# Performance work log

Hardware: AMD Instinct MI355X
Metric: run time of the kernel (lower is better)

The kernel has to match this reference:

```python
import jax, jax.numpy as jnp
import numpy as np

N, B, T, D = 4, 4, 512, 512
H, DK, DV = 8, 64, 64
LN_EPS = 1e-5


def setup_inputs() -> dict:
    key = jax.random.key(0)
    ks = jax.random.split(key, 5)
    s = 1.0 / np.sqrt(D)
    return {
        "x": jax.random.normal(ks[0], (N, B, T, D), jnp.float32),
        "Wq": jax.random.normal(ks[1], (D, H * DK), jnp.float32) * s,
        "bq": jnp.zeros((H * DK,), jnp.float32),
        "Wk": jax.random.normal(ks[2], (D, H * DK), jnp.float32) * s,
        "bk": jnp.zeros((H * DK,), jnp.float32),
        "Wv": jax.random.normal(ks[3], (D, H * DV), jnp.float32) * s,
        "bv": jnp.zeros((H * DV,), jnp.float32),
        "Wo": jax.random.normal(ks[4], (H * DV, D), jnp.float32) * (1.0 / np.sqrt(H * DV)),
        "bo": jnp.zeros((D,), jnp.float32),
        "gamma": jnp.ones((D,), jnp.float32),
        "beta": jnp.zeros((D,), jnp.float32),
    }


def reference(x, Wq, bq, Wk, bk, Wv, bv, Wo, bo, gamma, beta):
    # x: [N, B, T, D] -- N variables, each [B, T, D]
    n = x.shape[0]
    # Project once per variable (the torch code redundantly recomputes K/V per query var).
    q = (x @ Wq + bq).reshape(n, B, T, H, DK).transpose(0, 1, 3, 2, 4)  # [N,B,H,T,DK]
    k = (x @ Wk + bk).reshape(n, B, T, H, DK).transpose(0, 1, 3, 2, 4)  # [N,B,H,T,DK]
    v = (x @ Wv + bv).reshape(n, B, T, H, DV).transpose(0, 1, 3, 2, 4)  # [N,B,H,T,DV]
    # All-pairs attention: softmax over keys of EACH key-variable separately.
    scores = jnp.einsum('qbhtk,cbhsk->qcbhts', q, k) / np.sqrt(DK)  # [Nq,Nc,B,H,T,T]
    attn = jax.nn.softmax(scores, axis=-1)
    ctx = jnp.einsum('qcbhts,cbhsv->qcbhtv', attn, v)  # [Nq,Nc,B,H,T,DV]
    ctx = ctx.transpose(0, 1, 2, 4, 3, 5).reshape(n, n, B, T, H * DV)
    out = ctx @ Wo + bo                     # per-pair output projection
    out = out.sum(axis=1) / n               # average over key variables -> [N,B,T,D]
    res = x + out
    mu = res.mean(axis=-1, keepdims=True)
    var = res.var(axis=-1, keepdims=True)
    y = (res - mu) / jnp.sqrt(var + LN_EPS) * gamma + beta
    return y
```

## Files before the change

### kernel.cpp

```cpp
#include <hip/hip_runtime.h>


typedef __bf16 bf16x8 __attribute__((ext_vector_type(8)));
typedef __bf16 bf16x4 __attribute__((ext_vector_type(4)));
typedef short shortx4 __attribute__((ext_vector_type(4)));
typedef float floatx2 __attribute__((ext_vector_type(2)));
typedef float floatx4 __attribute__((ext_vector_type(4)));
typedef float floatx16 __attribute__((ext_vector_type(16)));
typedef unsigned short ushortx8 __attribute__((ext_vector_type(8)));
typedef unsigned int uintx4 __attribute__((ext_vector_type(4)));

static __device__ __forceinline__ unsigned short f2bf(float f) {
  union { __bf16 h; unsigned short u; } c; c.h = (__bf16)f; return c.u;
}
static __device__ __forceinline__ float bf2f(unsigned short u) {
  union { unsigned u32; float f; } c; c.u32 = ((unsigned)u) << 16; return c.f;
}
static __device__ __forceinline__ unsigned cvtpk(float a, float b) {
  unsigned r;
  asm("v_cvt_pk_bf16_f32 %0, %1, %2" : "=v"(r) : "v"(a), "v"(b));
  return r;
}

#define QSCALE 0.18033688011112042f
#define SHIFT2 (-17.312340489609306f)

__global__ __launch_bounds__(256) void prep(
    const float* __restrict__ Wq, const float* __restrict__ Wk,
    const float* __restrict__ Wv, const float* __restrict__ Wo,
    const float* __restrict__ x,
    unsigned short* __restrict__ wqkvT, unsigned short* __restrict__ woT,
    unsigned short* __restrict__ x_bf)
{
  const int bid = blockIdx.x;
  const int tid = threadIdx.x;
  if (bid < 256) {
    __shared__ unsigned short lds[64][65];
    const int z = bid >> 6, rest = bid & 63;
    const int k0 = (rest >> 3) * 64, n0 = (rest & 7) * 64;
    const float* W; unsigned short* T;
    if (z == 0)      { W = Wq; T = wqkvT; }
    else if (z == 1) { W = Wk; T = wqkvT + 262144; }
    else if (z == 2) { W = Wv; T = wqkvT + 524288; }
    else             { W = Wo; T = woT; }
    const int xx = tid & 63, yy = tid >> 6;
#pragma unroll
    for (int i = 0; i < 16; ++i) {
      const int row = yy * 16 + i;
      lds[row][xx] = f2bf(W[(size_t)(k0 + row) * 512 + n0 + xx]);
    }
    __syncthreads();
#pragma unroll
    for (int i = 0; i < 16; ++i) {
      const int nr = yy * 16 + i;
      T[(size_t)(n0 + nr) * 512 + k0 + xx] = lds[xx][nr];
    }
  } else {
    const int i = (bid - 256) * 256 + tid;
    const float4 a = ((const float4*)x)[i * 2];
    const float4 b = ((const float4*)x)[i * 2 + 1];
    ushortx8 o;
    o[0] = f2bf(a.x); o[1] = f2bf(a.y); o[2] = f2bf(a.z); o[3] = f2bf(a.w);
    o[4] = f2bf(b.x); o[5] = f2bf(b.y); o[6] = f2bf(b.z); o[7] = f2bf(b.w);
    *(ushortx8*)(x_bf + (size_t)i * 8) = o;
  }
}

__global__ __launch_bounds__(256) void gemm_qkv(
    const unsigned short* __restrict__ Xb,
    const unsigned short* __restrict__ BT,
    const float* __restrict__ bq, const float* __restrict__ bk,
    const float* __restrict__ bv,
    unsigned short* __restrict__ Qo, unsigned short* __restrict__ Ko,
    unsigned short* __restrict__ Vo)
{
  __shared__ __align__(16) unsigned short sbuf[18432];
  auto lA = (unsigned short (*)[72])sbuf;
  auto lB = (unsigned short (*)[72])(sbuf + 9216);
  const int tid  = threadIdx.x;
  const int wv   = tid >> 6, lane = tid & 63;
  const int quad = lane >> 4, l16 = lane & 15;
  const int wm = wv >> 1, wn = wv & 1;
  const int m0  = blockIdx.x * 128;
  const int n0g = blockIdx.y * 128;
  const int sel = n0g >> 9;
  const float* bias = (sel == 0) ? bq : (sel == 1) ? bk : bv;
  const float scale = (sel == 0) ? QSCALE : 1.0f;
  unsigned short* outp = (sel == 0) ? Qo : (sel == 1) ? Ko : Vo;

  floatx4 acc[4][4] = {};
  const int srow = tid >> 1, sc0 = (tid & 1) * 32;

  for (int kc = 0; kc < 512; kc += 64) {
    __syncthreads();
    const unsigned short* as = Xb + (size_t)(m0 + srow) * 512 + kc + sc0;
    const unsigned short* bs = BT + (size_t)(n0g + srow) * 512 + kc + sc0;
#pragma unroll
    for (int j = 0; j < 4; ++j) {
      *(bf16x8*)&lA[srow][sc0 + j * 8] = *(const bf16x8*)(as + j * 8);
      *(bf16x8*)&lB[srow][sc0 + j * 8] = *(const bf16x8*)(bs + j * 8);
    }
    __syncthreads();
    bf16x8 af[4][2];
#pragma unroll
    for (int ti = 0; ti < 4; ++ti) {
      af[ti][0] = *(const bf16x8*)&lA[wm * 64 + ti * 16 + l16][quad * 8];
      af[ti][1] = *(const bf16x8*)&lA[wm * 64 + ti * 16 + l16][32 + quad * 8];
    }
#pragma unroll
    for (int ni = 0; ni < 4; ++ni) {
      bf16x8 b0 = *(const bf16x8*)&lB[wn * 64 + ni * 16 + l16][quad * 8];
      bf16x8 b1 = *(const bf16x8*)&lB[wn * 64 + ni * 16 + l16][32 + quad * 8];
#pragma unroll
      for (int ti = 0; ti < 4; ++ti) {
        acc[ti][ni] = __builtin_amdgcn_mfma_f32_16x16x32_bf16(af[ti][0], b0, acc[ti][ni], 0, 0, 0);
        acc[ti][ni] = __builtin_amdgcn_mfma_f32_16x16x32_bf16(af[ti][1], b1, acc[ti][ni], 0, 0, 0);
      }
    }
  }

  __syncthreads();
  if (sel != 2) {
    auto tb = (unsigned short (*)[136])sbuf;
#pragma unroll
    for (int ni = 0; ni < 4; ++ni) {
      const int ncol = wn * 64 + ni * 16 + l16;
      const float bvv = bias[(n0g & 511) + ncol];
#pragma unroll
      for (int ti = 0; ti < 4; ++ti) {
        const int mrow = wm * 64 + ti * 16 + quad * 4;
#pragma unroll
        for (int r = 0; r < 4; ++r)
          tb[mrow + r][ncol] = f2bf((acc[ti][ni][r] + bvv) * scale);
      }
    }
    __syncthreads();
    const int mrow = tid >> 1, th = tid & 1;
    const int m = m0 + mrow;
    const int nb2 = m >> 9, t = m & 511;
    const int hh = ((n0g & 511) >> 6) + th;
    unsigned short* gdst = outp + ((size_t)(nb2 * 8 + hh) * 512 + t) * 64;
#pragma unroll
    for (int j = 0; j < 8; ++j)
      *(ushortx8*)(gdst + j * 8) = *(const ushortx8*)&tb[mrow][th * 64 + j * 8];
  } else {
    auto tb = (unsigned short (*)[136])sbuf;
#pragma unroll
    for (int ni = 0; ni < 4; ++ni) {
      const int n = (n0g & 511) + wn * 64 + ni * 16 + l16;
      const float bvv = bias[n];
      const int drow = wn * 64 + ni * 16 + l16;
#pragma unroll
      for (int ti = 0; ti < 4; ++ti) {
        const int tcol = wm * 64 + ti * 16 + quad * 4;
        shortx4 pk;
        pk[0] = (short)f2bf(acc[ti][ni][0] + bvv);
        pk[1] = (short)f2bf(acc[ti][ni][1] + bvv);
        pk[2] = (short)f2bf(acc[ti][ni][2] + bvv);
        pk[3] = (short)f2bf(acc[ti][ni][3] + bvv);
        *(shortx4*)&tb[drow][tcol] = pk;
      }
    }
    __syncthreads();
    const int drow = tid >> 1, th = tid & 1;
    const int n = (n0g & 511) + drow;
    const int hh = n >> 6, dk = n & 63;
    const int nb = m0 >> 9, tbase = (m0 & 511) + th * 64;
    unsigned short* gdst = outp + ((size_t)(nb * 8 + hh) * 64 + dk) * 512 + tbase;
#pragma unroll
    for (int j = 0; j < 8; ++j)
      *(ushortx8*)(gdst + j * 8) = *(const ushortx8*)&tb[drow][th * 64 + j * 8];
  }
}

__global__ __launch_bounds__(256) void gemm_out(
    const unsigned short* __restrict__ C0, const unsigned short* __restrict__ C1,
    const unsigned short* __restrict__ BT, unsigned short* __restrict__ Cout)
{
  __shared__ __align__(16) unsigned short sbuf[18432];
  auto lA = (unsigned short (*)[72])sbuf;
  auto lB = (unsigned short (*)[72])(sbuf + 9216);
  const int tid  = threadIdx.x;
  const int wv   = tid >> 6, lane = tid & 63;
  const int quad = lane >> 4, l16 = lane & 15;
  const int wm = wv >> 1, wn = wv & 1;
  const int m0 = blockIdx.x * 128, n0 = blockIdx.y * 128;

  floatx4 acc[4][4] = {};
  const int srow = tid >> 1, sc0 = (tid & 1) * 32;

  for (int kc = 0; kc < 512; kc += 64) {
    __syncthreads();
    const size_t aoff = (size_t)(m0 + srow) * 512 + kc + sc0;
    const unsigned short* bs = BT + (size_t)(n0 + srow) * 512 + kc + sc0;
#pragma unroll
    for (int j = 0; j < 4; ++j) {
      ushortx8 a0 = *(const ushortx8*)(C0 + aoff + j * 8);
      ushortx8 a1 = *(const ushortx8*)(C1 + aoff + j * 8);
      ushortx8 o;
#pragma unroll
      for (int e = 0; e < 8; ++e) o[e] = f2bf(bf2f(a0[e]) + bf2f(a1[e]));
      *(ushortx8*)&lA[srow][sc0 + j * 8] = o;
      *(bf16x8*)&lB[srow][sc0 + j * 8] = *(const bf16x8*)(bs + j * 8);
    }
    __syncthreads();
    bf16x8 af[4][2];
#pragma unroll
    for (int ti = 0; ti < 4; ++ti) {
      af[ti][0] = *(const bf16x8*)&lA[wm * 64 + ti * 16 + l16][quad * 8];
      af[ti][1] = *(const bf16x8*)&lA[wm * 64 + ti * 16 + l16][32 + quad * 8];
    }
#pragma unroll
    for (int ni = 0; ni < 4; ++ni) {
      bf16x8 b0 = *(const bf16x8*)&lB[wn * 64 + ni * 16 + l16][quad * 8];
      bf16x8 b1 = *(const bf16x8*)&lB[wn * 64 + ni * 16 + l16][32 + quad * 8];
#pragma unroll
      for (int ti = 0; ti < 4; ++ti) {
        acc[ti][ni] = __builtin_amdgcn_mfma_f32_16x16x32_bf16(af[ti][0], b0, acc[ti][ni], 0, 0, 0);
        acc[ti][ni] = __builtin_amdgcn_mfma_f32_16x16x32_bf16(af[ti][1], b1, acc[ti][ni], 0, 0, 0);
      }
    }
  }

  __syncthreads();
  auto tb = (unsigned short (*)[136])sbuf;
#pragma unroll
  for (int ni = 0; ni < 4; ++ni) {
    const int ncol = wn * 64 + ni * 16 + l16;
#pragma unroll
    for (int ti = 0; ti < 4; ++ti) {
      const int mrow = wm * 64 + ti * 16 + quad * 4;
#pragma unroll
      for (int r = 0; r < 4; ++r)
        tb[mrow + r][ncol] = f2bf(acc[ti][ni][r]);
    }
  }
  __syncthreads();
  const int mrow = tid >> 1, th = tid & 1;
  unsigned short* gdst = Cout + (size_t)(m0 + mrow) * 512 + n0 + th * 64;
#pragma unroll
  for (int j = 0; j < 8; ++j)
    *(ushortx8*)(gdst + j * 8) = *(const ushortx8*)&tb[mrow][th * 64 + j * 8];
}

__global__ __launch_bounds__(256) void flash_kernel(
    const unsigned short* __restrict__ Q,
    const unsigned short* __restrict__ K,
    const unsigned short* __restrict__ VT,
    unsigned short* __restrict__ CTX2)
{
  __shared__ __align__(16) unsigned short lK[2][64][72];
  __shared__ __align__(16) unsigned short lV[2][64][68];
  const int tid  = threadIdx.x;
  const int wv   = tid >> 6, lane = tid & 63;
  const int l32  = lane & 31, u = lane >> 5;

  const int lin  = blockIdx.x;
  const int xcd  = lin & 7, slot = lin >> 3;
  const int tile = slot & 3;
  const int nbh  = xcd * 16 + ((slot >> 2) & 15);
  const int cg   = slot >> 6;
  const int t0   = tile * 128;
  const int h = nbh & 7, nb = nbh >> 3, b = nb & 3;

  const unsigned short* qbase = Q + ((size_t)nbh * 512 + (t0 + wv * 32 + l32)) * 64;
  bf16x8 qf[4];
#pragma unroll
  for (int c16 = 0; c16 < 4; ++c16)
    qf[c16] = *(const bf16x8*)(qbase + c16 * 16 + u * 8);

  const int srow = tid >> 2, sc0 = (tid & 3) * 16;
  const unsigned short *kptr, *vptr;
  auto setptr = [&](int it) {
    const int c = cg * 2 + (it >> 3), s0 = (it & 7) * 64;
    const size_t kvbh = (size_t)((c * 4 + b) * 8 + h);
    kptr = K  + kvbh * (512 * 64) + (size_t)(s0 + srow) * 64 + sc0;
    vptr = VT + kvbh * (64 * 512) + (size_t)srow * 512 + s0 + sc0;
  };
  bf16x8 rk0, rk1, rv0, rv1;
  auto loadregs = [&]() {
    rk0 = *(const bf16x8*)kptr; rk1 = *(const bf16x8*)(kptr + 8);
    rv0 = *(const bf16x8*)vptr; rv1 = *(const bf16x8*)(vptr + 8);
  };
  auto writebuf = [&](int p) {
    *(bf16x8*)&lK[p][srow][sc0]     = rk0;
    *(bf16x8*)&lK[p][srow][sc0 + 8] = rk1;
    union { bf16x8 v8; bf16x4 v4[2]; } c0, c1;
    c0.v8 = rv0; c1.v8 = rv1;
    *(bf16x4*)&lV[p][srow][sc0]      = c0.v4[0];
    *(bf16x4*)&lV[p][srow][sc0 + 4]  = c0.v4[1];
    *(bf16x4*)&lV[p][srow][sc0 + 8]  = c1.v4[0];
    *(bf16x4*)&lV[p][srow][sc0 + 12] = c1.v4[1];
  };

  setptr(0); loadregs();
  writebuf(0);
  setptr(1); loadregs();
  __syncthreads();

  floatx16 ofin0 = {}, ofin1 = {};
  floatx16 oc0, oc1;
  floatx2 lac2;

  for (int it = 0; it < 16; ++it) {
    const int cur = it & 1;
    const int st = it & 7;
    if (st == 0) { oc0 = floatx16{}; oc1 = floatx16{}; lac2 = floatx2{}; }

    if (it < 15) writebuf(cur ^ 1);
    if (it < 14) { setptr(it + 2); loadregs(); }

    __builtin_amdgcn_s_setprio(1);
    floatx16 sacc0, sacc1;
#pragma unroll
    for (int r = 0; r < 16; ++r) { sacc0[r] = SHIFT2; sacc1[r] = SHIFT2; }
#pragma unroll
    for (int c16 = 0; c16 < 4; ++c16) {
      bf16x8 ak0 = *(const bf16x8*)&lK[cur][l32][c16 * 16 + u * 8];
      bf16x8 ak1 = *(const bf16x8*)&lK[cur][32 + l32][c16 * 16 + u * 8];
      sacc0 = __builtin_amdgcn_mfma_f32_32x32x16_bf16(ak0, qf[c16], sacc0, 0, 0, 0);
      sacc1 = __builtin_amdgcn_mfma_f32_32x32x16_bf16(ak1, qf[c16], sacc1, 0, 0, 0);
    }

#pragma unroll
    for (int sb = 0; sb < 2; ++sb) {
      const floatx16& sa = sb ? sacc1 : sacc0;
#pragma unroll
      for (int g = 0; g < 2; ++g) {
        float e[8];
#pragma unroll
        for (int j = 0; j < 8; ++j) e[j] = __builtin_amdgcn_exp2f(sa[8 * g + j]);
        floatx2 s01 = floatx2{e[0], e[1]} + floatx2{e[2], e[3]};
        floatx2 s23 = floatx2{e[4], e[5]} + floatx2{e[6], e[7]};
        lac2 += s01 + s23;
        union { unsigned u32[4]; bf16x8 b8; } pf;
        pf.u32[0] = cvtpk(e[0], e[1]);
        pf.u32[1] = cvtpk(e[2], e[3]);
        pf.u32[2] = cvtpk(e[4], e[5]);
        pf.u32[3] = cvtpk(e[6], e[7]);
        const int slA = sb * 32 + g * 16 + u * 4;
        union { shortx4 s4[2]; bf16x8 b8; } va, vb;
        va.s4[0] = *(const shortx4*)&lV[cur][l32][slA];
        va.s4[1] = *(const shortx4*)&lV[cur][l32][slA + 8];
        vb.s4[0] = *(const shortx4*)&lV[cur][32 + l32][slA];
        vb.s4[1] = *(const shortx4*)&lV[cur][32 + l32][slA + 8];
        oc0 = __builtin_amdgcn_mfma_f32_32x32x16_bf16(pf.b8, va.b8, oc0, 0, 0, 0);
        oc1 = __builtin_amdgcn_mfma_f32_32x32x16_bf16(pf.b8, vb.b8, oc1, 0, 0, 0);
      }
    }
    __builtin_amdgcn_s_setprio(0);

    if (st == 7) {
      float s = lac2[0] + lac2[1];
      s += __shfl_xor(s, 32);
      const float inv = 1.0f / s;
#pragma unroll
      for (int r = 0; r < 16; ++r) {
        const int trow = (r & 3) + 8 * (r >> 2) + 4 * u;
        const float invr = __shfl(inv, trow);
        ofin0[r] += oc0[r] * invr;
        ofin1[r] += oc1[r] * invr;
      }
    }
    __syncthreads();
  }

  unsigned short* outp = CTX2 + (size_t)cg * (8192 * 512);
  const int mbase = nb * 512 + t0 + wv * 32;
#pragma unroll
  for (int r = 0; r < 16; ++r) {
    const int trow = (r & 3) + 8 * (r >> 2) + 4 * u;
    const size_t rowoff = (size_t)(mbase + trow) * 512 + h * 64;
    outp[rowoff + l32]      = f2bf(ofin0[r]);
    outp[rowoff + 32 + l32] = f2bf(ofin1[r]);
  }
}

__global__ __launch_bounds__(256) void ln_kernel(
    const float* __restrict__ x, const unsigned short* __restrict__ tmpb,
    const float* __restrict__ bo, const float* __restrict__ gamma,
    const float* __restrict__ beta, float* __restrict__ out)
{
  const int wv   = threadIdx.x >> 6, lane = threadIdx.x & 63;
  const int row  = blockIdx.x * 4 + wv;
  const int col  = lane * 8;
  const size_t base = (size_t)row * 512 + col;
  const float4 x0 = *(const float4*)(x + base);
  const float4 x1 = *(const float4*)(x + base + 4);
  const ushortx8 t8 = *(const ushortx8*)(tmpb + base);
  const float4 b0 = *(const float4*)(bo + col);
  const float4 b1 = *(const float4*)(bo + col + 4);
  float r[8];
  r[0] = x0.x + 0.25f * bf2f(t8[0]) + b0.x;  r[1] = x0.y + 0.25f * bf2f(t8[1]) + b0.y;
  r[2] = x0.z + 0.25f * bf2f(t8[2]) + b0.z;  r[3] = x0.w + 0.25f * bf2f(t8[3]) + b0.w;
  r[4] = x1.x + 0.25f * bf2f(t8[4]) + b1.x;  r[5] = x1.y + 0.25f * bf2f(t8[5]) + b1.y;
  r[6] = x1.z + 0.25f * bf2f(t8[6]) + b1.z;  r[7] = x1.w + 0.25f * bf2f(t8[7]) + b1.w;
  float s = 0.f, sq = 0.f;
#pragma unroll
  for (int j = 0; j < 8; ++j) { s += r[j]; sq += r[j] * r[j]; }
#pragma unroll
  for (int off = 1; off < 64; off <<= 1) {
    s  += __shfl_xor(s, off);
    sq += __shfl_xor(sq, off);
  }
  const float mu  = s * (1.0f / 512.0f);
  const float var = sq * (1.0f / 512.0f) - mu * mu;
  const float inv = rsqrtf(var + 1e-5f);
  const float4 g0 = *(const float4*)(gamma + col);
  const float4 g1 = *(const float4*)(gamma + col + 4);
  const float4 be0 = *(const float4*)(beta + col);
  const float4 be1 = *(const float4*)(beta + col + 4);
  float4 o0, o1;
  o0.x = (r[0] - mu) * inv * g0.x + be0.x;  o0.y = (r[1] - mu) * inv * g0.y + be0.y;
  o0.z = (r[2] - mu) * inv * g0.z + be0.z;  o0.w = (r[3] - mu) * inv * g0.w + be0.w;
  o1.x = (r[4] - mu) * inv * g1.x + be1.x;  o1.y = (r[5] - mu) * inv * g1.y + be1.y;
  o1.z = (r[6] - mu) * inv * g1.z + be1.z;  o1.w = (r[7] - mu) * inv * g1.w + be1.w;
  *(float4*)(out + base)     = o0;
  *(float4*)(out + base + 4) = o1;
}

extern "C" void kernel_launch(void* const* d_in, const int* in_sizes, int n_in,
                              void* d_out, int out_size, void* d_ws, size_t ws_size,
                              hipStream_t stream) {
  const float* x     = (const float*)d_in[0];
  const float* Wq    = (const float*)d_in[1];
  const float* bq    = (const float*)d_in[2];
  const float* Wk    = (const float*)d_in[3];
  const float* bk    = (const float*)d_in[4];
  const float* Wv    = (const float*)d_in[5];
  const float* bv    = (const float*)d_in[6];
  const float* Wo    = (const float*)d_in[7];
  const float* bo    = (const float*)d_in[8];
  const float* gamma = (const float*)d_in[9];
  const float* beta  = (const float*)d_in[10];
  float* out = (float*)d_out;

  char* w = (char*)d_ws;
  unsigned short* q_bf  = (unsigned short*)(w);
  unsigned short* k_bf  = (unsigned short*)(w + (size_t)8  * 1024 * 1024);
  unsigned short* vt_bf = (unsigned short*)(w + (size_t)16 * 1024 * 1024);
  unsigned short* x_bf  = (unsigned short*)(w + (size_t)24 * 1024 * 1024);
  unsigned short* ctx2  = (unsigned short*)(w + (size_t)24 * 1024 * 1024);
  unsigned short* wqkvT = (unsigned short*)(w + (size_t)40 * 1024 * 1024);
  unsigned short* woT   = wqkvT + 786432;
  unsigned short* tmpb  = (unsigned short*)(w);

  prep<<<2304, 256, 0, stream>>>(Wq, Wk, Wv, Wo, x, wqkvT, woT, x_bf);
  gemm_qkv<<<dim3(64, 12), 256, 0, stream>>>(x_bf, wqkvT, bq, bk, bv,
                                             q_bf, k_bf, vt_bf);
  flash_kernel<<<1024, 256, 0, stream>>>(q_bf, k_bf, vt_bf, ctx2);
  gemm_out<<<dim3(64, 4), 256, 0, stream>>>(ctx2, ctx2 + (size_t)8192 * 512,
                                            woT, tmpb);
  ln_kernel<<<2048, 256, 0, stream>>>(x, tmpb, bo, gamma, beta, out);
}
```

Measured before the change: 185.5 us.

## Fuse output projection GEMM with residual add and LayerNorm

Replaces the separate output-projection GEMM and LayerNorm kernels with one kernel. Each 512-thread block computes a full 64-row by 512-column output tile into shared memory, then applies the residual, bias and LayerNorm directly. This removes the bf16 intermediate write and read and one kernel launch. In exchange the grid shrinks to 128 blocks, which leaves many CUs idle. The A-operand sum is also recomputed for each of the four column chunks.

```diff
diff --git a/kernel.cpp b/kernel.cpp
--- a/kernel.cpp
+++ b/kernel.cpp
@@ -171,76 +171,6 @@
     for (int j = 0; j < 8; ++j)
       *(ushortx8*)(gdst + j * 8) = *(const ushortx8*)&tb[drow][th * 64 + j * 8];
   }
-}
-
-__global__ __launch_bounds__(256) void gemm_out(
-    const unsigned short* __restrict__ C0, const unsigned short* __restrict__ C1,
-    const unsigned short* __restrict__ BT, unsigned short* __restrict__ Cout)
-{
-  __shared__ __align__(16) unsigned short sbuf[18432];
-  auto lA = (unsigned short (*)[72])sbuf;
-  auto lB = (unsigned short (*)[72])(sbuf + 9216);
-  const int tid  = threadIdx.x;
-  const int wv   = tid >> 6, lane = tid & 63;
-  const int quad = lane >> 4, l16 = lane & 15;
-  const int wm = wv >> 1, wn = wv & 1;
-  const int m0 = blockIdx.x * 128, n0 = blockIdx.y * 128;
-
-  floatx4 acc[4][4] = {};
-  const int srow = tid >> 1, sc0 = (tid & 1) * 32;
-
-  for (int kc = 0; kc < 512; kc += 64) {
-    __syncthreads();
-    const size_t aoff = (size_t)(m0 + srow) * 512 + kc + sc0;
-    const unsigned short* bs = BT + (size_t)(n0 + srow) * 512 + kc + sc0;
-#pragma unroll
-    for (int j = 0; j < 4; ++j) {
-      ushortx8 a0 = *(const ushortx8*)(C0 + aoff + j * 8);
-      ushortx8 a1 = *(const ushortx8*)(C1 + aoff + j * 8);
-      ushortx8 o;
-#pragma unroll
-      for (int e = 0; e < 8; ++e) o[e] = f2bf(bf2f(a0[e]) + bf2f(a1[e]));
-      *(ushortx8*)&lA[srow][sc0 + j * 8] = o;
-      *(bf16x8*)&lB[srow][sc0 + j * 8] = *(const bf16x8*)(bs + j * 8);
-    }
-    __syncthreads();
-    bf16x8 af[4][2];
-#pragma unroll
-    for (int ti = 0; ti < 4; ++ti) {
-      af[ti][0] = *(const bf16x8*)&lA[wm * 64 + ti * 16 + l16][quad * 8];
-      af[ti][1] = *(const bf16x8*)&lA[wm * 64 + ti * 16 + l16][32 + quad * 8];
-    }
-#pragma unroll
-    for (int ni = 0; ni < 4; ++ni) {
-      bf16x8 b0 = *(const bf16x8*)&lB[wn * 64 + ni * 16 + l16][quad * 8];
-      bf16x8 b1 = *(const bf16x8*)&lB[wn * 64 + ni * 16 + l16][32 + quad * 8];
-#pragma unroll
-      for (int ti = 0; ti < 4; ++ti) {
-        acc[ti][ni] = __builtin_amdgcn_mfma_f32_16x16x32_bf16(af[ti][0], b0, acc[ti][ni], 0, 0, 0);
-        acc[ti][ni] = __builtin_amdgcn_mfma_f32_16x16x32_bf16(af[ti][1], b1, acc[ti][ni], 0, 0, 0);
-      }
-    }
-  }
-
-  __syncthreads();
-  auto tb = (unsigned short (*)[136])sbuf;
-#pragma unroll
-  for (int ni = 0; ni < 4; ++ni) {
-    const int ncol = wn * 64 + ni * 16 + l16;
-#pragma unroll
-    for (int ti = 0; ti < 4; ++ti) {
-      const int mrow = wm * 64 + ti * 16 + quad * 4;
-#pragma unroll
-      for (int r = 0; r < 4; ++r)
-        tb[mrow + r][ncol] = f2bf(acc[ti][ni][r]);
-    }
-  }
-  __syncthreads();
-  const int mrow = tid >> 1, th = tid & 1;
-  unsigned short* gdst = Cout + (size_t)(m0 + mrow) * 512 + n0 + th * 64;
-#pragma unroll
-  for (int j = 0; j < 8; ++j)
-    *(ushortx8*)(gdst + j * 8) = *(const ushortx8*)&tb[mrow][th * 64 + j * 8];
 }
 
 __global__ __launch_bounds__(256) void flash_kernel(
@@ -376,47 +306,111 @@
   }
 }
 
-__global__ __launch_bounds__(256) void ln_kernel(
-    const float* __restrict__ x, const unsigned short* __restrict__ tmpb,
-    const float* __restrict__ bo, const float* __restrict__ gamma,
-    const float* __restrict__ beta, float* __restrict__ out)
+__global__ __launch_bounds__(512) void gemm_out_ln(
+    const unsigned short* __restrict__ C0, const unsigned short* __restrict__ C1,
+    const unsigned short* __restrict__ BT,
+    const float* __restrict__ x, const float* __restrict__ bo,
+    const float* __restrict__ gamma, const float* __restrict__ beta,
+    float* __restrict__ out)
 {
-  const int wv   = threadIdx.x >> 6, lane = threadIdx.x & 63;
-  const int row  = blockIdx.x * 4 + wv;
-  const int col  = lane * 8;
-  const size_t base = (size_t)row * 512 + col;
-  const float4 x0 = *(const float4*)(x + base);
-  const float4 x1 = *(const float4*)(x + base + 4);
-  const ushortx8 t8 = *(const ushortx8*)(tmpb + base);
+  __shared__ __align__(16) unsigned short outbuf[64][520];
+  __shared__ __align__(16) unsigned short lA[64][72];
+  __shared__ __align__(16) unsigned short lB[128][72];
+  const int tid  = threadIdx.x;
+  const int wv   = tid >> 6, lane = tid & 63;
+  const int quad = lane >> 4, l16 = lane & 15;
+  const int wm = wv >> 2, wn = wv & 3;
+  const int m0 = blockIdx.x * 64;
+
+  for (int j = 0; j < 4; ++j) {
+    const int n0 = j * 128;
+    floatx4 acc[2][2] = {};
+    for (int kc = 0; kc < 512; kc += 64) {
+      __syncthreads();
+      {
+        const int ar = tid >> 3, ac = (tid & 7) * 8;
+        const size_t aoff = (size_t)(m0 + ar) * 512 + kc + ac;
+        ushortx8 a0 = *(const ushortx8*)(C0 + aoff);
+        ushortx8 a1 = *(const ushortx8*)(C1 + aoff);
+        ushortx8 o;
+#pragma unroll
+        for (int e = 0; e < 8; ++e) o[e] = f2bf(bf2f(a0[e]) + bf2f(a1[e]));
+        *(ushortx8*)&lA[ar][ac] = o;
+        const int br = tid >> 2, bc = (tid & 3) * 16;
+        const unsigned short* bs = BT + (size_t)(n0 + br) * 512 + kc + bc;
+        *(bf16x8*)&lB[br][bc]     = *(const bf16x8*)(bs);
+        *(bf16x8*)&lB[br][bc + 8] = *(const bf16x8*)(bs + 8);
+      }
+      __syncthreads();
+      bf16x8 af[2][2];
+#pragma unroll
+      for (int ti = 0; ti < 2; ++ti) {
+        af[ti][0] = *(const bf16x8*)&lA[wm * 32 + ti * 16 + l16][quad * 8];
+        af[ti][1] = *(const bf16x8*)&lA[wm * 32 + ti * 16 + l16][32 + quad * 8];
+      }
+#pragma unroll
+      for (int ni = 0; ni < 2; ++ni) {
+        bf16x8 b0 = *(const bf16x8*)&lB[wn * 32 + ni * 16 + l16][quad * 8];
+        bf16x8 b1 = *(const bf16x8*)&lB[wn * 32 + ni * 16 + l16][32 + quad * 8];
+#pragma unroll
+        for (int ti = 0; ti < 2; ++ti) {
+          acc[ti][ni] = __builtin_amdgcn_mfma_f32_16x16x32_bf16(af[ti][0], b0, acc[ti][ni], 0, 0, 0);
+          acc[ti][ni] = __builtin_amdgcn_mfma_f32_16x16x32_bf16(af[ti][1], b1, acc[ti][ni], 0, 0, 0);
+        }
+      }
+    }
+#pragma unroll
+    for (int ni = 0; ni < 2; ++ni) {
+      const int ncol = n0 + wn * 32 + ni * 16 + l16;
+#pragma unroll
+      for (int ti = 0; ti < 2; ++ti) {
+        const int mrow = wm * 32 + ti * 16 + quad * 4;
+#pragma unroll
+        for (int r = 0; r < 4; ++r)
+          outbuf[mrow + r][ncol] = f2bf(acc[ti][ni][r]);
+      }
+    }
+  }
+  __syncthreads();
+
+  const int col = lane * 8;
   const float4 b0 = *(const float4*)(bo + col);
   const float4 b1 = *(const float4*)(bo + col + 4);
-  float r[8];
-  r[0] = x0.x + 0.25f * bf2f(t8[0]) + b0.x;  r[1] = x0.y + 0.25f * bf2f(t8[1]) + b0.y;
-  r[2] = x0.z + 0.25f * bf2f(t8[2]) + b0.z;  r[3] = x0.w + 0.25f * bf2f(t8[3]) + b0.w;
-  r[4] = x1.x + 0.25f * bf2f(t8[4]) + b1.x;  r[5] = x1.y + 0.25f * bf2f(t8[5]) + b1.y;
-  r[6] = x1.z + 0.25f * bf2f(t8[6]) + b1.z;  r[7] = x1.w + 0.25f * bf2f(t8[7]) + b1.w;
-  float s = 0.f, sq = 0.f;
-#pragma unroll
-  for (int j = 0; j < 8; ++j) { s += r[j]; sq += r[j] * r[j]; }
-#pragma unroll
-  for (int off = 1; off < 64; off <<= 1) {
-    s  += __shfl_xor(s, off);
-    sq += __shfl_xor(sq, off);
-  }
-  const float mu  = s * (1.0f / 512.0f);
-  const float var = sq * (1.0f / 512.0f) - mu * mu;
-  const float inv = rsqrtf(var + 1e-5f);
   const float4 g0 = *(const float4*)(gamma + col);
   const float4 g1 = *(const float4*)(gamma + col + 4);
   const float4 be0 = *(const float4*)(beta + col);
   const float4 be1 = *(const float4*)(beta + col + 4);
-  float4 o0, o1;
-  o0.x = (r[0] - mu) * inv * g0.x + be0.x;  o0.y = (r[1] - mu) * inv * g0.y + be0.y;
-  o0.z = (r[2] - mu) * inv * g0.z + be0.z;  o0.w = (r[3] - mu) * inv * g0.w + be0.w;
-  o1.x = (r[4] - mu) * inv * g1.x + be1.x;  o1.y = (r[5] - mu) * inv * g1.y + be1.y;
-  o1.z = (r[6] - mu) * inv * g1.z + be1.z;  o1.w = (r[7] - mu) * inv * g1.w + be1.w;
-  *(float4*)(out + base)     = o0;
-  *(float4*)(out + base + 4) = o1;
+#pragma unroll
+  for (int rr = 0; rr < 8; ++rr) {
+    const int row = wv * 8 + rr;
+    const size_t base = (size_t)(m0 + row) * 512 + col;
+    const float4 x0 = *(const float4*)(x + base);
+    const float4 x1 = *(const float4*)(x + base + 4);
+    const ushortx8 t8 = *(const ushortx8*)&outbuf[row][col];
+    float r[8];
+    r[0] = x0.x + 0.25f * bf2f(t8[0]) + b0.x;  r[1] = x0.y + 0.25f * bf2f(t8[1]) + b0.y;
+    r[2] = x0.z + 0.25f * bf2f(t8[2]) + b0.z;  r[3] = x0.w + 0.25f * bf2f(t8[3]) + b0.w;
+    r[4] = x1.x + 0.25f * bf2f(t8[4]) + b1.x;  r[5] = x1.y + 0.25f * bf2f(t8[5]) + b1.y;
+    r[6] = x1.z + 0.25f * bf2f(t8[6]) + b1.z;  r[7] = x1.w + 0.25f * bf2f(t8[7]) + b1.w;
+    float s = 0.f, sq = 0.f;
+#pragma unroll
+    for (int jj = 0; jj < 8; ++jj) { s += r[jj]; sq += r[jj] * r[jj]; }
+#pragma unroll
+    for (int off = 1; off < 64; off <<= 1) {
+      s  += __shfl_xor(s, off);
+      sq += __shfl_xor(sq, off);
+    }
+    const float mu  = s * (1.0f / 512.0f);
+    const float var = sq * (1.0f / 512.0f) - mu * mu;
+    const float inv = rsqrtf(var + 1e-5f);
+    float4 o0, o1;
+    o0.x = (r[0] - mu) * inv * g0.x + be0.x;  o0.y = (r[1] - mu) * inv * g0.y + be0.y;
+    o0.z = (r[2] - mu) * inv * g0.z + be0.z;  o0.w = (r[3] - mu) * inv * g0.w + be0.w;
+    o1.x = (r[4] - mu) * inv * g1.x + be1.x;  o1.y = (r[5] - mu) * inv * g1.y + be1.y;
+    o1.z = (r[6] - mu) * inv * g1.z + be1.z;  o1.w = (r[7] - mu) * inv * g1.w + be1.w;
+    *(float4*)(out + base)     = o0;
+    *(float4*)(out + base + 4) = o1;
+  }
 }
 
 extern "C" void kernel_launch(void* const* d_in, const int* in_sizes, int n_in,
@@ -443,13 +437,11 @@
   unsigned short* ctx2  = (unsigned short*)(w + (size_t)24 * 1024 * 1024);
   unsigned short* wqkvT = (unsigned short*)(w + (size_t)40 * 1024 * 1024);
   unsigned short* woT   = wqkvT + 786432;
-  unsigned short* tmpb  = (unsigned short*)(w);
 
   prep<<<2304, 256, 0, stream>>>(Wq, Wk, Wv, Wo, x, wqkvT, woT, x_bf);
   gemm_qkv<<<dim3(64, 12), 256, 0, stream>>>(x_bf, wqkvT, bq, bk, bv,
                                              q_bf, k_bf, vt_bf);
   flash_kernel<<<1024, 256, 0, stream>>>(q_bf, k_bf, vt_bf, ctx2);
-  gemm_out<<<dim3(64, 4), 256, 0, stream>>>(ctx2, ctx2 + (size_t)8192 * 512,
-                                            woT, tmpb);
-  ln_kernel<<<2048, 256, 0, stream>>>(x, tmpb, bo, gamma, beta, out);
-}
+  gemm_out_ln<<<128, 512, 0, stream>>>(ctx2, ctx2 + (size_t)8192 * 512,
+                                       woT, x, bo, gamma, beta, out);
+}
```

New measurement: 193.5 us. 1.04x slower.
